# Kernel tuning notes

Hardware: AMD Instinct MI355X
Metric: run time of the kernel (lower is better)

Reference implementation:

```python
import jax, jax.numpy as jnp
import numpy as np

N = 30000      # nodes
E = 400000     # edges
D_IN = 128     # input feature dim (== hidden)
HID = 128      # hidden_dim
H = 4          # attention heads
C = 128        # per-head out channels (concat=False -> averaged)
L = 3          # num_layers
G = 64         # graphs in batch
ED = 3         # edge_dim
EPS = 1e-5     # batchnorm eps
NEG = 0.2      # leaky relu slope


def setup_inputs() -> dict:
    key = jax.random.key(0)
    ks = jax.random.split(key, 24)
    s = 0.05
    inp = {
        'x': jax.random.normal(ks[0], (N, D_IN), jnp.float32),
        'edge_index': jax.random.randint(ks[1], (2, E), 0, N, dtype=jnp.int32),
        'edge_attr': jax.random.normal(ks[2], (E, ED), jnp.float32),
        'batch': jnp.sort(jax.random.randint(ks[3], (N,), 0, G, dtype=jnp.int32)),
        # GAT layer params (stacked over L layers; input_dim == HID so shapes match)
        'W': jax.random.normal(ks[4], (L, HID, H * C), jnp.float32) * s,
        'att_src': jax.random.normal(ks[5], (L, H, C), jnp.float32) * s,
        'att_dst': jax.random.normal(ks[6], (L, H, C), jnp.float32) * s,
        'We': jax.random.normal(ks[7], (L, ED, H * C), jnp.float32) * s,
        'att_e': jax.random.normal(ks[8], (L, H, C), jnp.float32) * s,
        'bias': jnp.zeros((L, C), jnp.float32),
        'gamma': jnp.ones((L, HID), jnp.float32),
        'beta': jnp.zeros((L, HID), jnp.float32),
        # node classifier MLP: 128 -> 64 -> 32 -> 2
        'nw1': jax.random.normal(ks[9], (HID, HID // 2), jnp.float32) * s,
        'nb1': jnp.zeros((HID // 2,), jnp.float32),
        'nw2': jax.random.normal(ks[10], (HID // 2, HID // 4), jnp.float32) * s,
        'nb2': jnp.zeros((HID // 4,), jnp.float32),
        'nw3': jax.random.normal(ks[11], (HID // 4, 2), jnp.float32) * s,
        'nb3': jnp.zeros((2,), jnp.float32),
        # graph classifier MLP: 256 -> 128 -> 64 -> 2
        'gw1': jax.random.normal(ks[12], (HID * 2, HID), jnp.float32) * s,
        'gb1': jnp.zeros((HID,), jnp.float32),
        'gw2': jax.random.normal(ks[13], (HID, HID // 2), jnp.float32) * s,
        'gb2': jnp.zeros((HID // 2,), jnp.float32),
        'gw3': jax.random.normal(ks[14], (HID // 2, 2), jnp.float32) * s,
        'gb3': jnp.zeros((2,), jnp.float32),
    }
    return inp


def _segment_softmax(a, seg, n):
    m = jax.ops.segment_max(a, seg, num_segments=n)
    ex = jnp.exp(a - m[seg])
    den = jax.ops.segment_sum(ex, seg, num_segments=n)
    return ex / den[seg]


def _gnn_forward(x, edge_index, edge_attr, batch, W, att_src, att_dst, We, att_e,
                 bias, gamma, beta, nw1, nb1, nw2, nb2, nw3, nb3,
                 gw1, gb1, gw2, gb2, gw3, gb3):
    src, dst = edge_index[0], edge_index[1]
    # add self loops (PyG default); edge_attr fill_value='mean' of incoming edges
    ones_e = jnp.ones((E,), x.dtype)
    deg = jax.ops.segment_sum(ones_e, dst, num_segments=N)
    ea_mean = jax.ops.segment_sum(edge_attr, dst, num_segments=N) / jnp.clip(deg, 1.0)[:, None]
    loops = jnp.arange(N, dtype=src.dtype)
    src_f = jnp.concatenate([src, loops])
    dst_f = jnp.concatenate([dst, loops])
    ea_f = jnp.concatenate([edge_attr, ea_mean], axis=0)  # [E+N, ED]

    h = x
    for i in range(L):
        xh = (h @ W[i]).reshape(N, H, C)                      # [N,H,C]
        a_s = (xh * att_src[i]).sum(-1)                       # [N,H]
        a_d = (xh * att_dst[i]).sum(-1)                       # [N,H]
        eh = (ea_f @ We[i]).reshape(-1, H, C)                 # [E+N,H,C]
        a_e = (eh * att_e[i]).sum(-1)                         # [E+N,H]
        alpha = jax.nn.leaky_relu(a_s[src_f] + a_d[dst_f] + a_e, NEG)
        alpha = _segment_softmax(alpha, dst_f, N)             # softmax over in-edges
        msg = xh[src_f] * alpha[..., None]                    # [E+N,H,C]
        out = jax.ops.segment_sum(msg, dst_f, num_segments=N) # [N,H,C]
        h = out.mean(axis=1) + bias[i]                        # concat=False head avg
        # BatchNorm1d (training-mode batch stats, biased var), then ReLU
        mu = h.mean(axis=0)
        var = ((h - mu) ** 2).mean(axis=0)
        h = (h - mu) / jnp.sqrt(var + EPS) * gamma[i] + beta[i]
        h = jax.nn.relu(h)
        # dropout: identity (eval mode)

    node_pred = jax.nn.relu(h @ nw1 + nb1)
    node_pred = jax.nn.relu(node_pred @ nw2 + nb2)
    node_pred = node_pred @ nw3 + nb3                         # [N,2]

    cnt = jax.ops.segment_sum(jnp.ones((N,), h.dtype), batch, num_segments=G)
    gmean = jax.ops.segment_sum(h, batch, num_segments=G) / jnp.clip(cnt, 1.0)[:, None]
    gmax = jax.ops.segment_max(h, batch, num_segments=G)
    gr = jnp.concatenate([gmean, gmax], axis=1)               # [G,256]
    graph_pred = jax.nn.relu(gr @ gw1 + gb1)
    graph_pred = jax.nn.relu(graph_pred @ gw2 + gb2)
    graph_pred = graph_pred @ gw3 + gb3                       # [G,2]
    return node_pred, graph_pred


def reference(x, edge_index, edge_attr, batch, W, att_src, att_dst, We, att_e,
              bias, gamma, beta, nw1, nb1, nw2, nb2, nw3, nb3,
              gw1, gb1, gw2, gb2, gw3, gb3):
    return _gnn_forward(x, edge_index, edge_attr, batch, W, att_src, att_dst,
                        We, att_e, bias, gamma, beta, nw1, nb1, nw2, nb2,
                        nw3, nb3, gw1, gb1, gw2, gb2, gw3, gb3)
```

## Files before the change

### kernel.cpp

```cpp
#include <hip/hip_runtime.h>
#include <float.h>

#define N_NODES 30000
#define N_EDGES 400000
#define N_TOT   430000
#define HID     128
#define NH      4
#define HC      512
#define NL      3
#define NG      64
#define NEG_SLOPE 0.2f
#define BN_EPS 1e-5f
#define POOL_CHUNK 32
#define LDA_PAD 136
#define SCAN_NB ((N_NODES + 1023) / 1024)

typedef __attribute__((ext_vector_type(8))) short bf16x8;
typedef __attribute__((ext_vector_type(4))) float f32x4;

__device__ __forceinline__ float atomAddF(float* p, float v) { return unsafeAtomicAdd(p, v); }

__device__ __forceinline__ unsigned encf(float x) {
  unsigned u = __float_as_uint(x);
  return (u & 0x80000000u) ? ~u : (u | 0x80000000u);
}
__device__ __forceinline__ float decf(unsigned u) {
  return (u & 0x80000000u) ? __uint_as_float(u ^ 0x80000000u) : __uint_as_float(~u);
}
__device__ __forceinline__ unsigned short f2bf(float f) {
  unsigned u = __float_as_uint(f);
  u += 0x7FFFu + ((u >> 16) & 1u);
  return (unsigned short)(u >> 16);
}
__device__ __forceinline__ float bf2f(unsigned short s) {
  return __uint_as_float(((unsigned)s) << 16);
}

__device__ __forceinline__ void accum_edge(float acc[4][4],
                                           float& d0, float& d1, float& d2, float& d3,
                                           float4 ex, ushort4 v) {
  float f0 = bf2f(v.x), f1 = bf2f(v.y), f2 = bf2f(v.z), f3 = bf2f(v.w);
  d0 += ex.x; d1 += ex.y; d2 += ex.z; d3 += ex.w;
  acc[0][0] = fmaf(ex.x, f0, acc[0][0]); acc[0][1] = fmaf(ex.x, f1, acc[0][1]);
  acc[0][2] = fmaf(ex.x, f2, acc[0][2]); acc[0][3] = fmaf(ex.x, f3, acc[0][3]);
  acc[1][0] = fmaf(ex.y, f0, acc[1][0]); acc[1][1] = fmaf(ex.y, f1, acc[1][1]);
  acc[1][2] = fmaf(ex.y, f2, acc[1][2]); acc[1][3] = fmaf(ex.y, f3, acc[1][3]);
  acc[2][0] = fmaf(ex.z, f0, acc[2][0]); acc[2][1] = fmaf(ex.z, f1, acc[2][1]);
  acc[2][2] = fmaf(ex.z, f2, acc[2][2]); acc[2][3] = fmaf(ex.z, f3, acc[2][3]);
  acc[3][0] = fmaf(ex.w, f0, acc[3][0]); acc[3][1] = fmaf(ex.w, f1, acc[3][1]);
  acc[3][2] = fmaf(ex.w, f2, acc[3][2]); acc[3][3] = fmaf(ex.w, f3, acc[3][3]);
}

__global__ void prep_att_kernel(const float* __restrict__ W, const float* __restrict__ att_src,
                                const float* __restrict__ att_dst, const float* __restrict__ We,
                                const float* __restrict__ att_e,
                                float* __restrict__ wsrc, float* __restrict__ wdst,
                                float* __restrict__ weatt) {
  int l = blockIdx.x, t = threadIdx.x;
  for (int h = 0; h < NH; ++h) {
    const float* as = att_src + (size_t)(l*NH + h)*HID;
    const float* ad = att_dst + (size_t)(l*NH + h)*HID;
    const float* wr = W + (size_t)(l*HID + t)*HC + h*HID;
    float s = 0.f, d = 0.f;
    for (int c = 0; c < HID; ++c) { float w = wr[c]; s += w*as[c]; d += w*ad[c]; }
    wsrc[(l*HID + t)*NH + h] = s;
    wdst[(l*HID + t)*NH + h] = d;
  }
  if (t < 3) {
    for (int h = 0; h < NH; ++h) {
      const float* ae = att_e + (size_t)(l*NH + h)*HID;
      const float* wr = We + (size_t)(l*3 + t)*HC + h*HID;
      float s = 0.f;
      for (int c = 0; c < HID; ++c) s += wr[c]*ae[c];
      weatt[(l*3 + t)*NH + h] = s;
    }
  }
}

__global__ void prep_wt2_kernel(const float* __restrict__ W, unsigned short* __restrict__ Wt2P) {
  int l = blockIdx.y;
  int idx = blockIdx.x*256 + threadIdx.x;
  int j    = idx & 7;
  int lane = (idx >> 3) & 63;
  int nf   = (idx >> 9) & 7;
  int kk   = idx >> 12;
  int co = nf*16 + (lane & 15);
  int k  = kk*32 + (lane >> 4)*8 + j;
  int h = k >> 7, ci = k & 127;
  Wt2P[(size_t)l*65536 + idx] = f2bf(0.25f * W[((size_t)l*HID + ci)*HC + h*128 + co]);
}

__global__ void prep_mlpw_kernel(const float* __restrict__ nw1, const float* __restrict__ nw2,
                                 unsigned short* __restrict__ wt1, unsigned short* __restrict__ wt2) {
  int t = blockIdx.x*256 + threadIdx.x;
  if (t < 64*128) {
    int n = t >> 7, k = t & 127;
    wt1[t] = f2bf(nw1[k*64 + n]);
  }
  if (t < 32*64) {
    int n = t >> 6, k = t & 63;
    wt2[t] = f2bf(nw2[k*32 + n]);
  }
}

__global__ void xconv_kernel(const float* __restrict__ x, unsigned short* __restrict__ hb16) {
  int i = blockIdx.x*256 + threadIdx.x;
  if (i >= N_NODES*HID/4) return;
  float4 v = *(const float4*)&x[(size_t)i*4];
  ushort4 o; o.x = f2bf(v.x); o.y = f2bf(v.y); o.z = f2bf(v.z); o.w = f2bf(v.w);
  *(ushort4*)&hb16[(size_t)i*4] = o;
}

__global__ void deg_kernel(const int* __restrict__ ei, int* __restrict__ degi) {
  int e = blockIdx.x*blockDim.x + threadIdx.x;
  if (e >= N_EDGES) return;
  atomicAdd(&degi[ei[N_EDGES + e]], 1);
}

__global__ __launch_bounds__(1024) void scan1_kernel(const int* __restrict__ degi,
                                                     int* __restrict__ rowptr,
                                                     int* __restrict__ fill,
                                                     int* __restrict__ blocksum) {
  __shared__ int sh[1024];
  int b = blockIdx.x, t = threadIdx.x;
  int idx = b*1024 + t;
  int d = (idx < N_NODES) ? degi[idx] : 0;
  sh[t] = d;
  __syncthreads();
  for (int off = 1; off < 1024; off <<= 1) {
    int v = (t >= off) ? sh[t - off] : 0;
    __syncthreads();
    sh[t] += v;
    __syncthreads();
  }
  if (idx < N_NODES) {
    rowptr[idx] = sh[t] - d;
    fill[idx] = 0;
  }
  if (t == 1023) blocksum[b] = sh[1023];
}

__global__ __launch_bounds__(1024) void scan2_kernel(const int* __restrict__ blocksum,
                                                     int* __restrict__ rowptr) {
  int b = blockIdx.x, t = threadIdx.x;
  int off = 0;
  for (int i = 0; i < b; ++i) off += blocksum[i];
  int idx = b*1024 + t;
  if (idx < N_NODES && b > 0) rowptr[idx] += off;
  if (b == SCAN_NB - 1 && t == 1023)
    rowptr[N_NODES] = off + blocksum[SCAN_NB - 1];
}

__global__ void csr_fill_kernel(const int* __restrict__ ei, const int* __restrict__ rowptr,
                                int* __restrict__ fill, int* __restrict__ csr_src,
                                int* __restrict__ csr_pos, int* __restrict__ csr_eid) {
  int e = blockIdx.x*blockDim.x + threadIdx.x;
  if (e >= N_EDGES) return;
  int s = ei[e], d = ei[N_EDGES + e];
  int pos = rowptr[d] + atomicAdd(&fill[d], 1);
  csr_src[pos] = s;
  csr_pos[e] = pos;
  csr_eid[pos] = e;
}

__global__ void easum_kernel(const int* __restrict__ rowptr, const int* __restrict__ csr_eid,
                             const float* __restrict__ ea, float* __restrict__ easum) {
  int n = blockIdx.x*256 + threadIdx.x;
  if (n >= N_NODES) return;
  int p0 = rowptr[n], p1 = rowptr[n+1];
  float s0 = 0.f, s1 = 0.f, s2 = 0.f;
  for (int p = p0; p < p1; ++p) {
    int e = csr_eid[p];
    s0 += ea[e*3+0]; s1 += ea[e*3+1]; s2 += ea[e*3+2];
  }
  easum[n*3+0] = s0; easum[n*3+1] = s1; easum[n*3+2] = s2;
}

__global__ __launch_bounds__(256) void asd_kernel(const float* __restrict__ hin,
                                                  const float* __restrict__ wsrcL,
                                                  const float* __restrict__ wdstL,
                                                  float* __restrict__ a_s, float* __restrict__ a_d) {
  int wid = (blockIdx.x*256 + threadIdx.x) >> 6;
  int lane = threadIdx.x & 63;
  if (wid >= N_NODES) return;
  float v0 = hin[(size_t)wid*HID + lane];
  float v1 = hin[(size_t)wid*HID + 64 + lane];
  float4 w0s = *(const float4*)&wsrcL[lane*4];
  float4 w1s = *(const float4*)&wsrcL[(64+lane)*4];
  float4 w0d = *(const float4*)&wdstL[lane*4];
  float4 w1d = *(const float4*)&wdstL[(64+lane)*4];
  float ps0 = v0*w0s.x + v1*w1s.x, ps1 = v0*w0s.y + v1*w1s.y;
  float ps2 = v0*w0s.z + v1*w1s.z, ps3 = v0*w0s.w + v1*w1s.w;
  float pd0 = v0*w0d.x + v1*w1d.x, pd1 = v0*w0d.y + v1*w1d.y;
  float pd2 = v0*w0d.z + v1*w1d.z, pd3 = v0*w0d.w + v1*w1d.w;
  #pragma unroll
  for (int off = 32; off > 0; off >>= 1) {
    ps0 += __shfl_xor(ps0, off); ps1 += __shfl_xor(ps1, off);
    ps2 += __shfl_xor(ps2, off); ps3 += __shfl_xor(ps3, off);
    pd0 += __shfl_xor(pd0, off); pd1 += __shfl_xor(pd1, off);
    pd2 += __shfl_xor(pd2, off); pd3 += __shfl_xor(pd3, off);
  }
  if (lane == 0) {
    *(float4*)&a_s[wid*4] = make_float4(ps0, ps1, ps2, ps3);
    *(float4*)&a_d[wid*4] = make_float4(pd0, pd1, pd2, pd3);
  }
}

__global__ void edge_ex_kernel(const int* __restrict__ ei, const float* __restrict__ ea,
                               const float* __restrict__ easum, const int* __restrict__ rowptr,
                               const float* __restrict__ a_s, const float* __restrict__ a_d,
                               const float* __restrict__ weattL, const int* __restrict__ csr_pos,
                               float* __restrict__ excsr, float* __restrict__ exself) {
  int e = blockIdx.x*blockDim.x + threadIdx.x;
  if (e >= N_TOT) return;
  int s, d; float e0, e1, e2;
  if (e < N_EDGES) {
    s = ei[e]; d = ei[N_EDGES + e];
    e0 = ea[e*3+0]; e1 = ea[e*3+1]; e2 = ea[e*3+2];
  } else {
    int n = e - N_EDGES; s = n; d = n;
    float dg = (float)(rowptr[n+1] - rowptr[n]);
    float inv = 1.f / fmaxf(dg, 1.f);
    e0 = easum[n*3+0]*inv; e1 = easum[n*3+1]*inv; e2 = easum[n*3+2]*inv;
  }
  float4 as4 = *(const float4*)&a_s[s*4];
  float4 ad4 = *(const float4*)&a_d[d*4];
  float4 w0 = *(const float4*)&weattL[0];
  float4 w1 = *(const float4*)&weattL[4];
  float4 w2 = *(const float4*)&weattL[8];
  float raw0 = as4.x + ad4.x + e0*w0.x + e1*w1.x + e2*w2.x;
  float raw1 = as4.y + ad4.y + e0*w0.y + e1*w1.y + e2*w2.y;
  float raw2 = as4.z + ad4.z + e0*w0.z + e1*w1.z + e2*w2.z;
  float raw3 = as4.w + ad4.w + e0*w0.w + e1*w1.w + e2*w2.w;
  raw0 = raw0 > 0.f ? raw0 : NEG_SLOPE*raw0;
  raw1 = raw1 > 0.f ? raw1 : NEG_SLOPE*raw1;
  raw2 = raw2 > 0.f ? raw2 : NEG_SLOPE*raw2;
  raw3 = raw3 > 0.f ? raw3 : NEG_SLOPE*raw3;
  float4 exv = make_float4(__expf(raw0), __expf(raw1), __expf(raw2), __expf(raw3));
  if (e < N_EDGES) {
    *(float4*)&excsr[(size_t)csr_pos[e]*4] = exv;
  } else {
    *(float4*)&exself[(size_t)(e - N_EDGES)*4] = exv;
  }
}

__global__ __launch_bounds__(256) void agg_kernel(const int* __restrict__ rowptr,
    const int* __restrict__ csr_src, const float* __restrict__ excsr,
    const float* __restrict__ exself, const unsigned short* __restrict__ hb16,
    unsigned short* __restrict__ g16, float* __restrict__ colsum, float* __restrict__ colsq) {
  if (blockIdx.x == 0) {
    int tt = threadIdx.x;
    if (tt < 128) colsum[tt] = 0.f;
    else colsq[tt-128] = 0.f;
  }
  int wid = (blockIdx.x*256 + threadIdx.x) >> 6;
  int lane = threadIdx.x & 63;
  if (wid >= N_NODES) return;
  int half = lane >> 5, li = lane & 31;
  int c0 = li * 4;
  int p0 = rowptr[wid], p1 = rowptr[wid+1];
  float acc[4][4] = {};
  float den0 = 0.f, den1 = 0.f, den2 = 0.f, den3 = 0.f;
  if (half == 0) {
    float4 ex = *(const float4*)&exself[(size_t)wid*4];
    ushort4 v = *(const ushort4*)&hb16[(size_t)wid*HID + c0];
    accum_edge(acc, den0, den1, den2, den3, ex, v);
  }
  int p = p0;
  for (; p + 8 <= p1; p += 8) {
    int base = p + half*4;
    int s0 = csr_src[base+0], s1 = csr_src[base+1], s2 = csr_src[base+2], s3 = csr_src[base+3];
    float4 e0 = *(const float4*)&excsr[(size_t)(base+0)*4];
    float4 e1 = *(const float4*)&excsr[(size_t)(base+1)*4];
    float4 e2 = *(const float4*)&excsr[(size_t)(base+2)*4];
    float4 e3 = *(const float4*)&excsr[(size_t)(base+3)*4];
    ushort4 v0 = *(const ushort4*)&hb16[(size_t)s0*HID + c0];
    ushort4 v1 = *(const ushort4*)&hb16[(size_t)s1*HID + c0];
    ushort4 v2 = *(const ushort4*)&hb16[(size_t)s2*HID + c0];
    ushort4 v3 = *(const ushort4*)&hb16[(size_t)s3*HID + c0];
    accum_edge(acc, den0, den1, den2, den3, e0, v0);
    accum_edge(acc, den0, den1, den2, den3, e1, v1);
    accum_edge(acc, den0, den1, den2, den3, e2, v2);
    accum_edge(acc, den0, den1, den2, den3, e3, v3);
  }
  for (; p + 2 <= p1; p += 2) {
    int pe = p + half;
    int s = csr_src[pe];
    float4 ex = *(const float4*)&excsr[(size_t)pe*4];
    ushort4 v = *(const ushort4*)&hb16[(size_t)s*HID + c0];
    accum_edge(acc, den0, den1, den2, den3, ex, v);
  }
  if (p < p1 && half == 0) {
    int s = csr_src[p];
    float4 ex = *(const float4*)&excsr[(size_t)p*4];
    ushort4 v = *(const ushort4*)&hb16[(size_t)s*HID + c0];
    accum_edge(acc, den0, den1, den2, den3, ex, v);
  }
  #pragma unroll
  for (int h = 0; h < 4; ++h)
    #pragma unroll
    for (int j = 0; j < 4; ++j)
      acc[h][j] += __shfl_xor(acc[h][j], 32);
  den0 += __shfl_xor(den0, 32); den1 += __shfl_xor(den1, 32);
  den2 += __shfl_xor(den2, 32); den3 += __shfl_xor(den3, 32);
  float inv[4] = {1.f/den0, 1.f/den1, 1.f/den2, 1.f/den3};
  #pragma unroll
  for (int k = 0; k < 2; ++k) {
    int h = half*2 + k;
    ushort4 o;
    o.x = f2bf(acc[h][0]*inv[h]); o.y = f2bf(acc[h][1]*inv[h]);
    o.z = f2bf(acc[h][2]*inv[h]); o.w = f2bf(acc[h][3]*inv[h]);
    *(ushort4*)&g16[(size_t)wid*HC + h*128 + c0] = o;
  }
}

#define MFMA16(a, b, c) __builtin_amdgcn_mfma_f32_16x16x32_bf16(a, b, c, 0, 0, 0)

__global__ __launch_bounds__(256) void gemm2_mfma_kernel(const unsigned short* __restrict__ g16,
                                                         const unsigned short* __restrict__ Wt2P,
                                                         float* __restrict__ C,
                                                         float* __restrict__ colsum,
                                                         float* __restrict__ colsq) {
  __shared__ unsigned short Bs[4*8*512];
  __shared__ float cs_s[128], cq_s[128];
  int m0 = blockIdx.x * 64;
  int t = threadIdx.x;
  int wave = t >> 6, lane = t & 63;
  int mbase = m0 + wave * 16;
  int lrow = lane & 15;
  if (t < 128) { cs_s[t] = 0.f; cq_s[t] = 0.f; }
  int arow = mbase + lrow;
  const unsigned short* arp = g16 + (size_t)(arow < N_NODES ? arow : 0)*HC + (lane >> 4)*8;
  f32x4 acc[8] = {};
  for (int ph = 0; ph < 4; ++ph) {
    const bf16x8* src = (const bf16x8*)(Wt2P + ph*16384);
    __syncthreads();
    #pragma unroll
    for (int i = 0; i < 8; ++i)
      *(bf16x8*)&Bs[(t + i*256)*8] = src[t + i*256];
    __syncthreads();
    #pragma unroll
    for (int kk = 0; kk < 4; ++kk) {
      bf16x8 a = *(const bf16x8*)&arp[(ph*4 + kk)*32];
      #pragma unroll
      for (int nf = 0; nf < 8; ++nf) {
        bf16x8 b = *(const bf16x8*)&Bs[(kk*8 + nf)*512 + lane*8];
        acc[nf] = MFMA16(a, b, acc[nf]);
      }
    }
  }
  int orow = (lane >> 4) * 4, ocol = lane & 15;
  #pragma unroll
  for (int nf = 0; nf < 8; ++nf) {
    float s = 0.f, q = 0.f;
    #pragma unroll
    for (int r = 0; r < 4; ++r) {
      int gm = mbase + orow + r;
      float v = acc[nf][r];
      if (gm < N_NODES) {
        C[(size_t)gm*HID + nf*16 + ocol] = v;
        s += v; q += v*v;
      }
    }
    atomicAdd(&cs_s[nf*16 + ocol], s);
    atomicAdd(&cq_s[nf*16 + ocol], q);
  }
  __syncthreads();
  if (t < 128) {
    atomAddF(&colsum[t], cs_s[t]);
    atomAddF(&colsq[t], cq_s[t]);
  }
}

__global__ __launch_bounds__(256) void bnasd_kernel(const float* __restrict__ hpre,
    const float* __restrict__ colsum, const float* __restrict__ colsq,
    const float* __restrict__ gammaL, const float* __restrict__ betaL,
    const float* __restrict__ wsrcL, const float* __restrict__ wdstL,
    unsigned short* __restrict__ hb16, float* __restrict__ a_s, float* __restrict__ a_d) {
  int wid = (blockIdx.x*256 + threadIdx.x) >> 6;
  int lane = threadIdx.x & 63;
  if (wid >= N_NODES) return;
  const float invn = 1.f / (float)N_NODES;
  float v0 = hpre[(size_t)wid*HID + lane];
  float v1 = hpre[(size_t)wid*HID + 64 + lane];
  float mu0 = colsum[lane]*invn, mu1 = colsum[64+lane]*invn;
  float var0 = fmaxf(colsq[lane]*invn - mu0*mu0, 0.f);
  float var1 = fmaxf(colsq[64+lane]*invn - mu1*mu1, 0.f);
  float sc0 = gammaL[lane]*rsqrtf(var0 + BN_EPS), sh0 = betaL[lane] - mu0*sc0;
  float sc1 = gammaL[64+lane]*rsqrtf(var1 + BN_EPS), sh1 = betaL[64+lane] - mu1*sc1;
  v0 = fmaxf(fmaf(v0, sc0, sh0), 0.f);
  v1 = fmaxf(fmaf(v1, sc1, sh1), 0.f);
  hb16[(size_t)wid*HID + lane] = f2bf(v0);
  hb16[(size_t)wid*HID + 64 + lane] = f2bf(v1);
  float4 w0s = *(const float4*)&wsrcL[lane*4];
  float4 w1s = *(const float4*)&wsrcL[(64+lane)*4];
  float4 w0d = *(const float4*)&wdstL[lane*4];
  float4 w1d = *(const float4*)&wdstL[(64+lane)*4];
  float ps0 = v0*w0s.x + v1*w1s.x, ps1 = v0*w0s.y + v1*w1s.y;
  float ps2 = v0*w0s.z + v1*w1s.z, ps3 = v0*w0s.w + v1*w1s.w;
  float pd0 = v0*w0d.x + v1*w1d.x, pd1 = v0*w0d.y + v1*w1d.y;
  float pd2 = v0*w0d.z + v1*w1d.z, pd3 = v0*w0d.w + v1*w1d.w;
  #pragma unroll
  for (int off = 32; off > 0; off >>= 1) {
    ps0 += __shfl_xor(ps0, off); ps1 += __shfl_xor(ps1, off);
    ps2 += __shfl_xor(ps2, off); ps3 += __shfl_xor(ps3, off);
    pd0 += __shfl_xor(pd0, off); pd1 += __shfl_xor(pd1, off);
    pd2 += __shfl_xor(pd2, off); pd3 += __shfl_xor(pd3, off);
  }
  if (lane == 0) {
    *(float4*)&a_s[wid*4] = make_float4(ps0, ps1, ps2, ps3);
    *(float4*)&a_d[wid*4] = make_float4(pd0, pd1, pd2, pd3);
  }
}

__global__ void bnfinal_kernel(const float* __restrict__ hpre,
                               const float* __restrict__ colsum, const float* __restrict__ colsq,
                               const float* __restrict__ gammaL, const float* __restrict__ betaL,
                               unsigned short* __restrict__ hb16) {
  int i = blockIdx.x*blockDim.x + threadIdx.x;
  if (i >= N_NODES*HID/4) return;
  int c4 = (i*4) & 127;
  const float invn = 1.f / (float)N_NODES;
  float4 v = *(const float4*)&hpre[(size_t)i*4];
  float4 cs = *(const float4*)&colsum[c4];
  float4 cq = *(const float4*)&colsq[c4];
  float4 gm = *(const float4*)&gammaL[c4];
  float4 bt = *(const float4*)&betaL[c4];
  float mu, var, sc, sh;
  mu = cs.x*invn; var = fmaxf(cq.x*invn - mu*mu, 0.f); sc = gm.x*rsqrtf(var + BN_EPS); sh = bt.x - mu*sc;
  v.x = fmaxf(fmaf(v.x, sc, sh), 0.f);
  mu = cs.y*invn; var = fmaxf(cq.y*invn - mu*mu, 0.f); sc = gm.y*rsqrtf(var + BN_EPS); sh = bt.y - mu*sc;
  v.y = fmaxf(fmaf(v.y, sc, sh), 0.f);
  mu = cs.z*invn; var = fmaxf(cq.z*invn - mu*mu, 0.f); sc = gm.z*rsqrtf(var + BN_EPS); sh = bt.z - mu*sc;
  v.z = fmaxf(fmaf(v.z, sc, sh), 0.f);
  mu = cs.w*invn; var = fmaxf(cq.w*invn - mu*mu, 0.f); sc = gm.w*rsqrtf(var + BN_EPS); sh = bt.w - mu*sc;
  v.w = fmaxf(fmaf(v.w, sc, sh), 0.f);
  ushort4 o; o.x = f2bf(v.x); o.y = f2bf(v.y); o.z = f2bf(v.z); o.w = f2bf(v.w);
  *(ushort4*)&hb16[(size_t)i*4] = o;
}

__global__ __launch_bounds__(256) void nodemlp_kernel(const unsigned short* __restrict__ h16,
    const unsigned short* __restrict__ wt1, const float* __restrict__ b1,
    const unsigned short* __restrict__ wt2, const float* __restrict__ b2,
    const float* __restrict__ w3, const float* __restrict__ b3,
    float* __restrict__ out,
    float* __restrict__ gsum, float* __restrict__ gcnt, unsigned* __restrict__ gmaxenc) {
  __shared__ unsigned short As[128 * LDA_PAD];
  __shared__ unsigned short L1s[128 * 72];
  __shared__ float L2s[128 * 33];
  int m0 = blockIdx.x * 128;
  int t = threadIdx.x;
  if (blockIdx.x == 0) {
    for (int i = t; i < NG*HID; i += 256) { gsum[i] = 0.f; gmaxenc[i] = 0x00800000u; }
    if (t < NG) gcnt[t] = 0.f;
  }
  #pragma unroll
  for (int i = 0; i < 8; ++i) {
    int idx = t + i*256;
    int row = idx >> 4, k8 = (idx & 15) * 8;
    int gm = m0 + row;
    bf16x8 v = {};
    if (gm < N_NODES) v = *(const bf16x8*)&h16[(size_t)gm*HID + k8];
    *(bf16x8*)&As[row*LDA_PAD + k8] = v;
  }
  __syncthreads();
  int wave = t >> 6, lane = t & 63;
  int mbase = wave * 32;
  int lrow = lane & 15, lk = (lane >> 4) * 8;
  int orow = (lane >> 4) * 4, ocol = lane & 15;
  f32x4 acc[2][4] = {};
  #pragma unroll
  for (int ks = 0; ks < 4; ++ks) {
    int k0 = ks * 32;
    bf16x8 a0 = *(const bf16x8*)&As[(mbase + lrow)*LDA_PAD + k0 + lk];
    bf16x8 a1 = *(const bf16x8*)&As[(mbase + 16 + lrow)*LDA_PAD + k0 + lk];
    #pragma unroll
    for (int nf = 0; nf < 4; ++nf) {
      bf16x8 b = *(const bf16x8*)&wt1[(size_t)(nf*16 + lrow)*HID + k0 + lk];
      acc[0][nf] = MFMA16(a0, b, acc[0][nf]);
      acc[1][nf] = MFMA16(a1, b, acc[1][nf]);
    }
  }
  #pragma unroll
  for (int mf = 0; mf < 2; ++mf)
    #pragma unroll
    for (int nf = 0; nf < 4; ++nf) {
      float bb = b1[nf*16 + ocol];
      #pragma unroll
      for (int r = 0; r < 4; ++r)
        L1s[(mbase + mf*16 + orow + r)*72 + nf*16 + ocol] = f2bf(fmaxf(acc[mf][nf][r] + bb, 0.f));
    }
  __syncthreads();
  f32x4 acc2[2][2] = {};
  #pragma unroll
  for (int ks = 0; ks < 2; ++ks) {
    int k0 = ks * 32;
    bf16x8 a0 = *(const bf16x8*)&L1s[(mbase + lrow)*72 + k0 + lk];
    bf16x8 a1 = *(const bf16x8*)&L1s[(mbase + 16 + lrow)*72 + k0 + lk];
    #pragma unroll
    for (int nf = 0; nf < 2; ++nf) {
      bf16x8 b = *(const bf16x8*)&wt2[(size_t)(nf*16 + lrow)*64 + k0 + lk];
      acc2[0][nf] = MFMA16(a0, b, acc2[0][nf]);
      acc2[1][nf] = MFMA16(a1, b, acc2[1][nf]);
    }
  }
  #pragma unroll
  for (int mf = 0; mf < 2; ++mf)
    #pragma unroll
    for (int nf = 0; nf < 2; ++nf) {
      float bb = b2[nf*16 + ocol];
      #pragma unroll
      for (int r = 0; r < 4; ++r)
        L2s[(mbase + mf*16 + orow + r)*33 + nf*16 + ocol] = fmaxf(acc2[mf][nf][r] + bb, 0.f);
    }
  __syncthreads();
  {
    int node = t >> 1, j = t & 1;
    int gm = m0 + node;
    if (gm < N_NODES) {
      float accv = b3[j];
      #pragma unroll
      for (int k = 0; k < 32; ++k)
        accv = fmaf(L2s[node*33 + k], w3[k*2 + j], accv);
      out[(size_t)gm*2 + j] = accv;
    }
  }
}

__global__ __launch_bounds__(128) void pool_seg_kernel(const unsigned short* __restrict__ h16,
                                                       const int* __restrict__ batch,
                                                       float* __restrict__ gsum,
                                                       unsigned* __restrict__ gmaxenc,
                                                       float* __restrict__ gcnt) {
  int t = threadIdx.x;
  int r0 = blockIdx.x * POOL_CHUNK;
  int rend = min(r0 + POOL_CHUNK, N_NODES);
  if (r0 >= N_NODES) return;
  int gcur = batch[r0];
  float s = 0.f, m = -FLT_MAX;
  int cnt = 0;
  for (int r = r0; r < rend; ++r) {
    int g = batch[r];
    if (g != gcur) {
      atomAddF(&gsum[gcur*HID + t], s);
      atomicMax(&gmaxenc[gcur*HID + t], encf(m));
      if (t == 0) atomAddF(&gcnt[gcur], (float)cnt);
      gcur = g; s = 0.f; m = -FLT_MAX; cnt = 0;
    }
    float v = bf2f(h16[(size_t)r*HID + t]);
    s += v; m = fmaxf(m, v);
    ++cnt;
  }
  atomAddF(&gsum[gcur*HID + t], s);
  atomicMax(&gmaxenc[gcur*HID + t], encf(m));
  if (t == 0) atomAddF(&gcnt[gcur], (float)cnt);
}

__global__ __launch_bounds__(128) void graphmlp_kernel(const float* __restrict__ gsum,
    const unsigned* __restrict__ gmaxenc, const float* __restrict__ gcnt,
    const float* __restrict__ gw1, const float* __restrict__ gb1,
    const float* __restrict__ gw2, const float* __restrict__ gb2,
    const float* __restrict__ gw3, const float* __restrict__ gb3,
    float* __restrict__ out) {
  __shared__ float gr[256], h1[128], h2[64];
  int g = blockIdx.x, t = threadIdx.x;
  float cnt = fmaxf(gcnt[g], 1.f);
  gr[t] = gsum[g*HID + t] / cnt;
  gr[128 + t] = decf(gmaxenc[g*HID + t]);
  __syncthreads();
  float acc = gb1[t];
  for (int k = 0; k < 256; ++k) acc += gr[k]*gw1[k*HID + t];
  h1[t] = fmaxf(acc, 0.f);
  __syncthreads();
  if (t < 64) {
    float a2 = gb2[t];
    for (int k = 0; k < 128; ++k) a2 += h1[k]*gw2[k*64 + t];
    h2[t] = fmaxf(a2, 0.f);
  }
  __syncthreads();
  if (t < 2) {
    float a3 = gb3[t];
    for (int k = 0; k < 64; ++k) a3 += h2[k]*gw3[k*2 + t];
    out[N_NODES*2 + g*2 + t] = a3;
  }
}

extern "C" void kernel_launch(void* const* d_in, const int* in_sizes, int n_in,
                              void* d_out, int out_size, void* d_ws, size_t ws_size,
                              hipStream_t stream) {
  (void)in_sizes; (void)n_in; (void)out_size; (void)ws_size;
  const float* x       = (const float*)d_in[0];
  const int*   ei      = (const int*)d_in[1];
  const float* ea      = (const float*)d_in[2];
  const int*   batch   = (const int*)d_in[3];
  const float* W       = (const float*)d_in[4];
  const float* att_src = (const float*)d_in[5];
  const float* att_dst = (const float*)d_in[6];
  const float* We      = (const float*)d_in[7];
  const float* att_e   = (const float*)d_in[8];
  const float* gamma   = (const float*)d_in[10];
  const float* beta    = (const float*)d_in[11];
  const float* nw1 = (const float*)d_in[12]; const float* nb1 = (const float*)d_in[13];
  const float* nw2 = (const float*)d_in[14]; const float* nb2 = (const float*)d_in[15];
  const float* nw3 = (const float*)d_in[16]; const float* nb3 = (const float*)d_in[17];
  const float* gw1 = (const float*)d_in[18]; const float* gb1 = (const float*)d_in[19];
  const float* gw2 = (const float*)d_in[20]; const float* gb2 = (const float*)d_in[21];
  const float* gw3 = (const float*)d_in[22]; const float* gb3 = (const float*)d_in[23];
  float* out = (float*)d_out;

  float* p = (float*)d_ws;
  unsigned short* g16 = (unsigned short*)p; p += (size_t)N_NODES*HC/2;
  unsigned short* hb16= (unsigned short*)p; p += (size_t)N_NODES*HID/2;
  float* hnext = p; p += (size_t)N_NODES*HID;
  float* excsr = p; p += (size_t)N_EDGES*NH;
  float* exself= p; p += (size_t)N_NODES*NH;
  float* a_s   = p; p += (size_t)N_NODES*NH;
  float* a_d   = p; p += (size_t)N_NODES*NH;
  float* easum = p; p += (size_t)N_NODES*3;
  float* wsrc  = p; p += NL*HID*NH;
  float* wdst  = p; p += NL*HID*NH;
  float* weatt = p; p += NL*3*NH;
  float* colsum= p; p += HID;
  float* colsq = p; p += HID;
  float* gsum  = p; p += NG*HID;
  float* gcnt  = p; p += NG;
  unsigned* gmaxenc = (unsigned*)p; p += NG*HID;
  int* degi    = (int*)p; p += N_NODES;
  int* rowptr  = (int*)p; p += (N_NODES + 1);
  int* fill    = (int*)p; p += N_NODES;
  int* blocksum= (int*)p; p += SCAN_NB;
  int* csr_src = (int*)p; p += N_EDGES;
  int* csr_pos = (int*)p; p += N_EDGES;
  int* csr_eid = (int*)p; p += N_EDGES;
  unsigned short* wt2  = (unsigned short*)p; p += NL*HID*HC/2;
  unsigned short* mw1  = (unsigned short*)p; p += 64*128/2;
  unsigned short* mw2  = (unsigned short*)p; p += 32*64/2;

  hipMemsetAsync(degi, 0, (size_t)N_NODES*sizeof(int), stream);
  prep_att_kernel<<<NL, 128, 0, stream>>>(W, att_src, att_dst, We, att_e, wsrc, wdst, weatt);
  prep_wt2_kernel<<<dim3(65536/256, NL), 256, 0, stream>>>(W, wt2);
  prep_mlpw_kernel<<<32, 256, 0, stream>>>(nw1, nw2, mw1, mw2);
  xconv_kernel<<<(N_NODES*HID/4+255)/256, 256, 0, stream>>>(x, hb16);
  deg_kernel<<<(N_EDGES+255)/256, 256, 0, stream>>>(ei, degi);
  scan1_kernel<<<SCAN_NB, 1024, 0, stream>>>(degi, rowptr, fill, blocksum);
  scan2_kernel<<<SCAN_NB, 1024, 0, stream>>>(blocksum, rowptr);
  csr_fill_kernel<<<(N_EDGES+255)/256, 256, 0, stream>>>(ei, rowptr, fill, csr_src, csr_pos, csr_eid);
  easum_kernel<<<(N_NODES+255)/256, 256, 0, stream>>>(rowptr, csr_eid, ea, easum);
  asd_kernel<<<(N_NODES*64)/256, 256, 0, stream>>>(x, wsrc, wdst, a_s, a_d);

  for (int l = 0; l < NL; ++l) {
    edge_ex_kernel<<<(N_TOT+255)/256, 256, 0, stream>>>(ei, ea, easum, rowptr, a_s, a_d,
                                                        weatt + l*3*NH, csr_pos, excsr, exself);
    agg_kernel<<<(N_NODES*64+255)/256, 256, 0, stream>>>(rowptr, csr_src, excsr, exself, hb16, g16,
                                                         colsum, colsq);
    gemm2_mfma_kernel<<<(N_NODES+63)/64, 256, 0, stream>>>(g16, wt2 + (size_t)l*65536,
                                                           hnext, colsum, colsq);
    if (l < NL-1) {
      bnasd_kernel<<<(N_NODES*64)/256, 256, 0, stream>>>(hnext, colsum, colsq,
                                                         gamma + l*HID, beta + l*HID,
                                                         wsrc + (l+1)*HID*NH, wdst + (l+1)*HID*NH,
                                                         hb16, a_s, a_d);
    } else {
      bnfinal_kernel<<<(N_NODES*HID/4+255)/256, 256, 0, stream>>>(hnext, colsum, colsq,
                                                                  gamma + l*HID, beta + l*HID, hb16);
    }
  }

  nodemlp_kernel<<<(N_NODES+127)/128, 256, 0, stream>>>(hb16, mw1, nb1, mw2, nb2, nw3, nb3, out,
                                                        gsum, gcnt, gmaxenc);
  pool_seg_kernel<<<(N_NODES + POOL_CHUNK - 1)/POOL_CHUNK, 128, 0, stream>>>(hb16, batch, gsum, gmaxenc, gcnt);
  graphmlp_kernel<<<NG, 128, 0, stream>>>(gsum, gmaxenc, gcnt, gw1, gb1, gw2, gb2, gw3, gb3, out);
}
```

Before: 435.5 us.

## Split aggregation into two column-half passes with four edge lanes per wave

The per-node aggregation kernel is split into two launches, each covering 64 of the 128 feature columns. Each wave now processes four edges at once, 16 lanes per edge, instead of two edges with 32 lanes each. The intent is more parallelism in the gather loop and a smaller per-pass gathered footprint for better cache hit rates. In exchange, edge indices and attention weights are read twice, there is an extra launch, and the shuffle reduction gains a step.

```diff
diff --git a/kernel.cpp b/kernel.cpp
--- a/kernel.cpp
+++ b/kernel.cpp
@@ -244,74 +244,80 @@
   }
 }
 
-__global__ __launch_bounds__(256) void agg_kernel(const int* __restrict__ rowptr,
+__global__ __launch_bounds__(256) void agg_half_kernel(const int* __restrict__ rowptr,
     const int* __restrict__ csr_src, const float* __restrict__ excsr,
     const float* __restrict__ exself, const unsigned short* __restrict__ hb16,
-    unsigned short* __restrict__ g16, float* __restrict__ colsum, float* __restrict__ colsq) {
-  if (blockIdx.x == 0) {
+    unsigned short* __restrict__ g16, float* __restrict__ colsum, float* __restrict__ colsq,
+    int coff) {
+  if (coff == 0 && blockIdx.x == 0) {
     int tt = threadIdx.x;
     if (tt < 128) colsum[tt] = 0.f;
-    else colsq[tt-128] = 0.f;
+    else if (tt < 256) colsq[tt-128] = 0.f;
   }
   int wid = (blockIdx.x*256 + threadIdx.x) >> 6;
   int lane = threadIdx.x & 63;
   if (wid >= N_NODES) return;
-  int half = lane >> 5, li = lane & 31;
-  int c0 = li * 4;
+  int q = lane >> 4, li = lane & 15;
+  int c0 = coff + li*4;
   int p0 = rowptr[wid], p1 = rowptr[wid+1];
   float acc[4][4] = {};
   float den0 = 0.f, den1 = 0.f, den2 = 0.f, den3 = 0.f;
-  if (half == 0) {
+  if (q == 0) {
     float4 ex = *(const float4*)&exself[(size_t)wid*4];
     ushort4 v = *(const ushort4*)&hb16[(size_t)wid*HID + c0];
     accum_edge(acc, den0, den1, den2, den3, ex, v);
   }
   int p = p0;
   for (; p + 8 <= p1; p += 8) {
-    int base = p + half*4;
-    int s0 = csr_src[base+0], s1 = csr_src[base+1], s2 = csr_src[base+2], s3 = csr_src[base+3];
-    float4 e0 = *(const float4*)&excsr[(size_t)(base+0)*4];
-    float4 e1 = *(const float4*)&excsr[(size_t)(base+1)*4];
-    float4 e2 = *(const float4*)&excsr[(size_t)(base+2)*4];
-    float4 e3 = *(const float4*)&excsr[(size_t)(base+3)*4];
-    ushort4 v0 = *(const ushort4*)&hb16[(size_t)s0*HID + c0];
-    ushort4 v1 = *(const ushort4*)&hb16[(size_t)s1*HID + c0];
-    ushort4 v2 = *(const ushort4*)&hb16[(size_t)s2*HID + c0];
-    ushort4 v3 = *(const ushort4*)&hb16[(size_t)s3*HID + c0];
-    accum_edge(acc, den0, den1, den2, den3, e0, v0);
-    accum_edge(acc, den0, den1, den2, den3, e1, v1);
-    accum_edge(acc, den0, den1, den2, den3, e2, v2);
-    accum_edge(acc, den0, den1, den2, den3, e3, v3);
-  }
-  for (; p + 2 <= p1; p += 2) {
-    int pe = p + half;
+    int pa = p + q, pb = p + 4 + q;
+    int sa = csr_src[pa], sb = csr_src[pb];
+    float4 ea = *(const float4*)&excsr[(size_t)pa*4];
+    float4 eb = *(const float4*)&excsr[(size_t)pb*4];
+    ushort4 va = *(const ushort4*)&hb16[(size_t)sa*HID + c0];
+    ushort4 vb = *(const ushort4*)&hb16[(size_t)sb*HID + c0];
+    accum_edge(acc, den0, den1, den2, den3, ea, va);
+    accum_edge(acc, den0, den1, den2, den3, eb, vb);
+  }
+  for (; p + 4 <= p1; p += 4) {
+    int pe = p + q;
     int s = csr_src[pe];
     float4 ex = *(const float4*)&excsr[(size_t)pe*4];
     ushort4 v = *(const ushort4*)&hb16[(size_t)s*HID + c0];
     accum_edge(acc, den0, den1, den2, den3, ex, v);
   }
-  if (p < p1 && half == 0) {
-    int s = csr_src[p];
-    float4 ex = *(const float4*)&excsr[(size_t)p*4];
+  if (p + q < p1) {
+    int pe = p + q;
+    int s = csr_src[pe];
+    float4 ex = *(const float4*)&excsr[(size_t)pe*4];
     ushort4 v = *(const ushort4*)&hb16[(size_t)s*HID + c0];
     accum_edge(acc, den0, den1, den2, den3, ex, v);
   }
   #pragma unroll
   for (int h = 0; h < 4; ++h)
     #pragma unroll
-    for (int j = 0; j < 4; ++j)
+    for (int j = 0; j < 4; ++j) {
+      acc[h][j] += __shfl_xor(acc[h][j], 16);
       acc[h][j] += __shfl_xor(acc[h][j], 32);
-  den0 += __shfl_xor(den0, 32); den1 += __shfl_xor(den1, 32);
-  den2 += __shfl_xor(den2, 32); den3 += __shfl_xor(den3, 32);
-  float inv[4] = {1.f/den0, 1.f/den1, 1.f/den2, 1.f/den3};
-  #pragma unroll
-  for (int k = 0; k < 2; ++k) {
-    int h = half*2 + k;
-    ushort4 o;
-    o.x = f2bf(acc[h][0]*inv[h]); o.y = f2bf(acc[h][1]*inv[h]);
-    o.z = f2bf(acc[h][2]*inv[h]); o.w = f2bf(acc[h][3]*inv[h]);
-    *(ushort4*)&g16[(size_t)wid*HC + h*128 + c0] = o;
-  }
+    }
+  den0 += __shfl_xor(den0, 16); den0 += __shfl_xor(den0, 32);
+  den1 += __shfl_xor(den1, 16); den1 += __shfl_xor(den1, 32);
+  den2 += __shfl_xor(den2, 16); den2 += __shfl_xor(den2, 32);
+  den3 += __shfl_xor(den3, 16); den3 += __shfl_xor(den3, 32);
+  ushort4 o;
+  if (q == 0) {
+    float iv = 1.f/den0;
+    o.x=f2bf(acc[0][0]*iv); o.y=f2bf(acc[0][1]*iv); o.z=f2bf(acc[0][2]*iv); o.w=f2bf(acc[0][3]*iv);
+  } else if (q == 1) {
+    float iv = 1.f/den1;
+    o.x=f2bf(acc[1][0]*iv); o.y=f2bf(acc[1][1]*iv); o.z=f2bf(acc[1][2]*iv); o.w=f2bf(acc[1][3]*iv);
+  } else if (q == 2) {
+    float iv = 1.f/den2;
+    o.x=f2bf(acc[2][0]*iv); o.y=f2bf(acc[2][1]*iv); o.z=f2bf(acc[2][2]*iv); o.w=f2bf(acc[2][3]*iv);
+  } else {
+    float iv = 1.f/den3;
+    o.x=f2bf(acc[3][0]*iv); o.y=f2bf(acc[3][1]*iv); o.z=f2bf(acc[3][2]*iv); o.w=f2bf(acc[3][3]*iv);
+  }
+  *(ushort4*)&g16[(size_t)wid*HC + q*128 + c0] = o;
 }
 
 #define MFMA16(a, b, c) __builtin_amdgcn_mfma_f32_16x16x32_bf16(a, b, c, 0, 0, 0)
@@ -651,8 +657,10 @@
   for (int l = 0; l < NL; ++l) {
     edge_ex_kernel<<<(N_TOT+255)/256, 256, 0, stream>>>(ei, ea, easum, rowptr, a_s, a_d,
                                                         weatt + l*3*NH, csr_pos, excsr, exself);
-    agg_kernel<<<(N_NODES*64+255)/256, 256, 0, stream>>>(rowptr, csr_src, excsr, exself, hb16, g16,
-                                                         colsum, colsq);
+    agg_half_kernel<<<(N_NODES*64+255)/256, 256, 0, stream>>>(rowptr, csr_src, excsr, exself,
+                                                              hb16, g16, colsum, colsq, 0);
+    agg_half_kernel<<<(N_NODES*64+255)/256, 256, 0, stream>>>(rowptr, csr_src, excsr, exself,
+                                                              hb16, g16, colsum, colsq, 64);
     gemm2_mfma_kernel<<<(N_NODES+63)/64, 256, 0, stream>>>(g16, wt2 + (size_t)l*65536,
                                                            hnext, colsum, colsq);
     if (l < NL-1) {
```

Result: slower. 448.9 us (+3.1%).
